# Kernel optimization log

Hardware: AMD Instinct MI355X
Metric: run time of the kernel (lower is better)

The kernel has to match this reference:

```python
import jax, jax.numpy as jnp
import numpy as np


def setup_inputs() -> dict:
    key = jax.random.key(0)
    k1, k2 = jax.random.split(key)
    B, D = 8192, 768
    M, K, dsub = 96, 256, 8  # subvector_num, 2**subvector_bits, emb_size // subvector_num
    vecs = jax.random.normal(k1, (B, D), dtype=jnp.float32)
    # matches nn.Parameter(...).uniform_(-0.1, 0.1)
    codebook = jax.random.uniform(k2, (M, K, dsub), dtype=jnp.float32, minval=-0.1, maxval=0.1)
    return {"vecs": vecs, "codebook": codebook}


def reference(vecs, codebook):
    B = vecs.shape[0]
    M, K, dsub = codebook.shape
    v = vecs.reshape(B, M, dsub)
    # code_selection: proba = -||v - c||^2, computed via expansion to avoid the
    # (B, M, K, dsub) broadcast intermediate: -(||v||^2 - 2 v.c + ||c||^2)
    v2 = jnp.sum(v * v, axis=-1, keepdims=True)       # (B, M, 1)
    c2 = jnp.sum(codebook * codebook, axis=-1)        # (M, K)
    vc = jnp.einsum('bmd,mkd->bmk', v, codebook)      # (B, M, K)
    proba = 2.0 * vc - v2 - c2[None]                  # (B, M, K)
    assign = jax.nn.softmax(proba, axis=-1)
    # STEstimator: hard one-hot forward, soft-assign gradient
    hard = jax.nn.one_hot(jnp.argmax(assign, axis=-1), K, dtype=assign.dtype)
    ste = assign + jax.lax.stop_gradient(hard - assign)
    # quantized_vecs: (B, M, 1, K) @ (M, K, dsub) -> (B, M, dsub) -> (B, D)
    q = jnp.einsum('bmk,mkd->bmd', ste, codebook)
    return q.reshape(B, M * dsub)
```

## Files before the change

### kernel.cpp

```cpp
#include <hip/hip_runtime.h>

namespace {
constexpr int kB = 8192;
constexpr int kD = 768;
constexpr int kM = 96;
constexpr int kK = 256;
constexpr int kDS = 8;
constexpr int kThreads = 256;
constexpr int kBPT = 4;
constexpr int kBT = kThreads * kBPT;
}

__device__ __forceinline__ float tree8_sq(float4 a, float4 b) {
    float q0 = __fmul_rn(a.x, a.x), q1 = __fmul_rn(a.y, a.y);
    float q2 = __fmul_rn(a.z, a.z), q3 = __fmul_rn(a.w, a.w);
    float q4 = __fmul_rn(b.x, b.x), q5 = __fmul_rn(b.y, b.y);
    float q6 = __fmul_rn(b.z, b.z), q7 = __fmul_rn(b.w, b.w);
    return __fadd_rn(__fadd_rn(__fadd_rn(q0, q1), __fadd_rn(q2, q3)),
                     __fadd_rn(__fadd_rn(q4, q5), __fadd_rn(q6, q7)));
}

__global__ __launch_bounds__(kThreads)
void pq_argmax_kernel(const float* __restrict__ vecs,
                      const float* __restrict__ cb,
                      float* __restrict__ out) {
    __shared__ float s_cb[kK * kDS];
    __shared__ float s_c2[kK];

    const int tid = threadIdx.x;
    const int m  = blockIdx.x % kM;
    const int bt = blockIdx.x / kM;

    {
        const float4* src = reinterpret_cast<const float4*>(cb) + (size_t)m * (kK * kDS / 4);
        float4 a = src[2 * tid + 0];
        float4 b = src[2 * tid + 1];
        reinterpret_cast<float4*>(s_cb)[2 * tid + 0] = a;
        reinterpret_cast<float4*>(s_cb)[2 * tid + 1] = b;
        s_c2[tid] = tree8_sq(a, b);
    }
    __syncthreads();

    const int b0 = bt * kBT + tid;

    float v[kBPT][kDS];
    float v2[kBPT];
#pragma unroll
    for (int j = 0; j < kBPT; ++j) {
        const float* vr = vecs + (size_t)(b0 + j * kThreads) * kD + m * kDS;
        float4 a = reinterpret_cast<const float4*>(vr)[0];
        float4 b = reinterpret_cast<const float4*>(vr)[1];
        v[j][0] = a.x; v[j][1] = a.y; v[j][2] = a.z; v[j][3] = a.w;
        v[j][4] = b.x; v[j][5] = b.y; v[j][6] = b.z; v[j][7] = b.w;
        v2[j] = tree8_sq(a, b);
    }

    float best[kBPT];
    int   bestk[kBPT];
#pragma unroll
    for (int j = 0; j < kBPT; ++j) { best[j] = -3.402823466e38f; bestk[j] = 0; }

#pragma unroll 4
    for (int k = 0; k < kK; ++k) {
        float4 ca  = reinterpret_cast<const float4*>(s_cb)[2 * k + 0];
        float4 cbv = reinterpret_cast<const float4*>(s_cb)[2 * k + 1];
        float  c2k = s_c2[k];
#pragma unroll
        for (int j = 0; j < kBPT; ++j) {
            float acc = __fmul_rn(v[j][0], ca.x);
            acc = __fadd_rn(acc, __fmul_rn(v[j][1], ca.y));
            acc = __fadd_rn(acc, __fmul_rn(v[j][2], ca.z));
            acc = __fadd_rn(acc, __fmul_rn(v[j][3], ca.w));
            acc = __fadd_rn(acc, __fmul_rn(v[j][4], cbv.x));
            acc = __fadd_rn(acc, __fmul_rn(v[j][5], cbv.y));
            acc = __fadd_rn(acc, __fmul_rn(v[j][6], cbv.z));
            acc = __fadd_rn(acc, __fmul_rn(v[j][7], cbv.w));
            float p = __fsub_rn(__fsub_rn(__fmul_rn(2.0f, acc), v2[j]), c2k);
            bool gt = p > best[j];
            best[j]  = gt ? p : best[j];
            bestk[j] = gt ? k : bestk[j];
        }
    }

#pragma unroll
    for (int j = 0; j < kBPT; ++j) {
        const float4* q = reinterpret_cast<const float4*>(s_cb) + 2 * bestk[j];
        float4* o = reinterpret_cast<float4*>(out + (size_t)(b0 + j * kThreads) * kD + m * kDS);
        o[0] = q[0];
        o[1] = q[1];
    }
}

extern "C" void kernel_launch(void* const* d_in, const int* in_sizes, int n_in,
                              void* d_out, int out_size, void* d_ws, size_t ws_size,
                              hipStream_t stream) {
    const float* vecs = (const float*)d_in[0];
    const float* cb   = (const float*)d_in[1];
    float* out = (float*)d_out;

    dim3 grid(kM * (kB / kBT));
    pq_argmax_kernel<<<grid, kThreads, 0, stream>>>(vecs, cb, out);
}
```

Baseline: 136.7 us.

## Compute code scores with fp16 split-precision MFMA and exact fp32 rescoring of near-ties

```diff
diff --git a/kernel.cpp b/kernel.cpp
--- a/kernel.cpp
+++ b/kernel.cpp
@@ -1,14 +1,20 @@
 #include <hip/hip_runtime.h>
+#include <hip/hip_fp16.h>
+
+typedef __attribute__((ext_vector_type(8))) _Float16 half8;
+typedef __attribute__((ext_vector_type(4))) float f32x4;
 
 namespace {
-constexpr int kB = 8192;
-constexpr int kD = 768;
-constexpr int kM = 96;
-constexpr int kK = 256;
-constexpr int kDS = 8;
+constexpr int kMsub = 96;
+constexpr int kK    = 256;
+constexpr int kDS   = 8;
+constexpr int kD    = 768;
 constexpr int kThreads = 256;
-constexpr int kBPT = 4;
-constexpr int kBT = kThreads * kBPT;
+constexpr int kWaves = 4;
+constexpr int kBPI  = 16;
+constexpr int kIters = 8;
+constexpr int kBPB  = kWaves * kBPI * kIters;
+constexpr float kEPS = 0.048f;
 }
 
 __device__ __forceinline__ float tree8_sq(float4 a, float4 b) {
@@ -20,74 +26,184 @@
                      __fadd_rn(__fadd_rn(q4, q5), __fadd_rn(q6, q7)));
 }
 
+__device__ __forceinline__ uint pkh(__half a, __half b) {
+    return (uint)__half_as_ushort(a) | ((uint)__half_as_ushort(b) << 16);
+}
+__device__ __forceinline__ uint pk2(float a, float b) {
+    return pkh(__float2half_rn(a), __float2half_rn(b));
+}
+union U4H8 { uint4 u; half8 h; };
+__device__ __forceinline__ half8 as_h8(uint4 u) { U4H8 x; x.u = u; return x.h; }
+
 __global__ __launch_bounds__(kThreads)
-void pq_argmax_kernel(const float* __restrict__ vecs,
-                      const float* __restrict__ cb,
-                      float* __restrict__ out) {
-    __shared__ float s_cb[kK * kDS];
-    __shared__ float s_c2[kK];
-
-    const int tid = threadIdx.x;
-    const int m  = blockIdx.x % kM;
-    const int bt = blockIdx.x / kM;
+void pq_mfma_kernel(const float* __restrict__ vecs,
+                    const float* __restrict__ cbg,
+                    float* __restrict__ out) {
+    __shared__ uint4  s_cbh[kK];
+    __shared__ uint4  s_cbl[kK];
+    __shared__ uint4  s_cbq[kK];
+    __shared__ uint   s_c2hl[kK];
+    __shared__ float  s_c2[kK];
+    __shared__ float4 s_cb[kK][2];
+    __shared__ float4 s_v[kWaves][kBPI][2];
+    __shared__ __align__(16) uint2 s_vh[kWaves][kBPI][2];
+    __shared__ __align__(16) uint2 s_vl[kWaves][kBPI][2];
+    __shared__ float s_v2[kWaves][kBPI];
+    __shared__ int   s_win[kWaves][kBPI];
+
+    const int tid  = threadIdx.x;
+    const int lane = tid & 63;
+    const int w    = tid >> 6;
+    const int m    = blockIdx.x % kMsub;
+    const int bt   = blockIdx.x / kMsub;
+    const int g    = lane >> 4;
+    const int c15  = lane & 15;
 
     {
-        const float4* src = reinterpret_cast<const float4*>(cb) + (size_t)m * (kK * kDS / 4);
-        float4 a = src[2 * tid + 0];
-        float4 b = src[2 * tid + 1];
-        reinterpret_cast<float4*>(s_cb)[2 * tid + 0] = a;
-        reinterpret_cast<float4*>(s_cb)[2 * tid + 1] = b;
-        s_c2[tid] = tree8_sq(a, b);
+        const int k = tid;
+        const float4* cr = reinterpret_cast<const float4*>(cbg + ((size_t)m * kK + k) * kDS);
+        float4 c0 = cr[0], c1 = cr[1];
+        s_cb[k][0] = c0; s_cb[k][1] = c1;
+        float c2 = tree8_sq(c0, c1);
+        s_c2[k] = c2;
+        float c2s = -128.0f * c2;
+        __half nh = __float2half_rn(c2s);
+        __half nl = __float2half_rn(c2s - __half2float(nh));
+        s_c2hl[k] = pkh(nh, nl);
+        float e[8] = {c0.x, c0.y, c0.z, c0.w, c1.x, c1.y, c1.z, c1.w};
+        uint hh[4], ll[4], qq[4];
+#pragma unroll
+        for (int i = 0; i < 4; ++i) {
+            float a = 256.0f * e[2*i], b = 256.0f * e[2*i+1];
+            __half ha = __float2half_rn(a), hb = __float2half_rn(b);
+            hh[i] = pkh(ha, hb);
+            ll[i] = pk2(a - __half2float(ha), b - __half2float(hb));
+            qq[i] = pk2(0.125f * e[2*i], 0.125f * e[2*i+1]);
+        }
+        s_cbh[k] = make_uint4(hh[0], hh[1], hh[2], hh[3]);
+        s_cbl[k] = make_uint4(ll[0], ll[1], ll[2], ll[3]);
+        s_cbq[k] = make_uint4(qq[0], qq[1], qq[2], qq[3]);
     }
     __syncthreads();
 
-    const int b0 = bt * kBT + tid;
-
-    float v[kBPT][kDS];
-    float v2[kBPT];
-#pragma unroll
-    for (int j = 0; j < kBPT; ++j) {
-        const float* vr = vecs + (size_t)(b0 + j * kThreads) * kD + m * kDS;
-        float4 a = reinterpret_cast<const float4*>(vr)[0];
-        float4 b = reinterpret_cast<const float4*>(vr)[1];
-        v[j][0] = a.x; v[j][1] = a.y; v[j][2] = a.z; v[j][3] = a.w;
-        v[j][4] = b.x; v[j][5] = b.y; v[j][6] = b.z; v[j][7] = b.w;
-        v2[j] = tree8_sq(a, b);
+    half8 A[16];
+#pragma unroll
+    for (int t = 0; t < 16; ++t) {
+        const int code = t * 16 + c15;
+        uint4 raw;
+        if (g == 0)      raw = s_cbh[code];
+        else if (g == 1) raw = s_cbl[code];
+        else if (g == 2) raw = s_cbq[code];
+        else             raw = make_uint4(s_c2hl[code], 0u, 0u, 0u);
+        A[t] = as_h8(raw);
     }
-
-    float best[kBPT];
-    int   bestk[kBPT];
-#pragma unroll
-    for (int j = 0; j < kBPT; ++j) { best[j] = -3.402823466e38f; bestk[j] = 0; }
-
-#pragma unroll 4
-    for (int k = 0; k < kK; ++k) {
-        float4 ca  = reinterpret_cast<const float4*>(s_cb)[2 * k + 0];
-        float4 cbv = reinterpret_cast<const float4*>(s_cb)[2 * k + 1];
-        float  c2k = s_c2[k];
-#pragma unroll
-        for (int j = 0; j < kBPT; ++j) {
-            float acc = __fmul_rn(v[j][0], ca.x);
-            acc = __fadd_rn(acc, __fmul_rn(v[j][1], ca.y));
-            acc = __fadd_rn(acc, __fmul_rn(v[j][2], ca.z));
-            acc = __fadd_rn(acc, __fmul_rn(v[j][3], ca.w));
-            acc = __fadd_rn(acc, __fmul_rn(v[j][4], cbv.x));
-            acc = __fadd_rn(acc, __fmul_rn(v[j][5], cbv.y));
-            acc = __fadd_rn(acc, __fmul_rn(v[j][6], cbv.z));
-            acc = __fadd_rn(acc, __fmul_rn(v[j][7], cbv.w));
-            float p = __fsub_rn(__fsub_rn(__fmul_rn(2.0f, acc), v2[j]), c2k);
-            bool gt = p > best[j];
-            best[j]  = gt ? p : best[j];
-            bestk[j] = gt ? k : bestk[j];
-        }
-    }
-
-#pragma unroll
-    for (int j = 0; j < kBPT; ++j) {
-        const float4* q = reinterpret_cast<const float4*>(s_cb) + 2 * bestk[j];
-        float4* o = reinterpret_cast<float4*>(out + (size_t)(b0 + j * kThreads) * kD + m * kDS);
-        o[0] = q[0];
-        o[1] = q[1];
+    const f32x4 zz = {0.0f, 0.0f, 0.0f, 0.0f};
+
+    for (int it = 0; it < kIters; ++it) {
+        const size_t bg0 = (size_t)bt * kBPB + (size_t)it * (kWaves * kBPI) + (size_t)w * kBPI;
+
+        float4 vown;
+        if (lane < 32) {
+            const int h = g;
+            const float4* vp = reinterpret_cast<const float4*>(
+                vecs + (bg0 + c15) * kD + (size_t)m * kDS) + h;
+            vown = *vp;
+            s_v[w][c15][h] = vown;
+            __half h0 = __float2half_rn(vown.x), h1 = __float2half_rn(vown.y);
+            __half h2 = __float2half_rn(vown.z), h3 = __float2half_rn(vown.w);
+            uint2 vhp = { pkh(h0, h1), pkh(h2, h3) };
+            uint2 vlp = { pk2(2048.0f * (vown.x - __half2float(h0)),
+                              2048.0f * (vown.y - __half2float(h1))),
+                          pk2(2048.0f * (vown.z - __half2float(h2)),
+                              2048.0f * (vown.w - __half2float(h3))) };
+            s_vh[w][c15][h] = vhp;
+            s_vl[w][c15][h] = vlp;
+        }
+        if (lane < 16) {
+            float4 vpart = s_v[w][c15][1];
+            s_v2[w][c15] = tree8_sq(vown, vpart);
+        }
+
+        half8 B;
+        {
+            uint4 raw;
+            if (g == 3) raw = make_uint4(0x3C003C00u, 0u, 0u, 0u);
+            else {
+                const uint4* p = (g == 2)
+                    ? reinterpret_cast<const uint4*>(&s_vl[w][c15][0])
+                    : reinterpret_cast<const uint4*>(&s_vh[w][c15][0]);
+                raw = *p;
+            }
+            B = as_h8(raw);
+        }
+        f32x4 D[16];
+#pragma unroll
+        for (int t = 0; t < 16; ++t)
+            D[t] = __builtin_amdgcn_mfma_f32_16x16x32_f16(A[t], B, zz, 0, 0, 0);
+
+        float m1 = -3.402823466e38f;
+#pragma unroll
+        for (int t = 0; t < 16; ++t)
+            m1 = fmaxf(m1, fmaxf(fmaxf(D[t].x, D[t].y), fmaxf(D[t].z, D[t].w)));
+        float gmax = fmaxf(m1, __shfl_xor(m1, 16));
+        gmax = fmaxf(gmax, __shfl_xor(gmax, 32));
+        const float thr = gmax - kEPS;
+
+        int cnt = 0, idx = 0;
+#pragma unroll
+        for (int t = 0; t < 16; ++t) {
+            { bool ge = D[t].x >= thr; cnt += ge ? 1 : 0; idx = ge ? (t*16 + g*4 + 0) : idx; }
+            { bool ge = D[t].y >= thr; cnt += ge ? 1 : 0; idx = ge ? (t*16 + g*4 + 1) : idx; }
+            { bool ge = D[t].z >= thr; cnt += ge ? 1 : 0; idx = ge ? (t*16 + g*4 + 2) : idx; }
+            { bool ge = D[t].w >= thr; cnt += ge ? 1 : 0; idx = ge ? (t*16 + g*4 + 3) : idx; }
+        }
+        int cnt4 = cnt + __shfl_xor(cnt, 16);
+        cnt4 += __shfl_xor(cnt4, 32);
+
+        if (cnt4 == 1) {
+            if (cnt == 1) s_win[w][c15] = idx;
+        } else {
+            float4 va = s_v[w][c15][0], vb = s_v[w][c15][1];
+            const float v2 = s_v2[w][c15];
+            float vr[8] = {va.x, va.y, va.z, va.w, vb.x, vb.y, vb.z, vb.w};
+            auto exactP = [&](int code) -> float {
+                float4 ca = s_cb[code][0], cc = s_cb[code][1];
+                float acc = __fmul_rn(vr[0], ca.x);
+                acc = __fadd_rn(acc, __fmul_rn(vr[1], ca.y));
+                acc = __fadd_rn(acc, __fmul_rn(vr[2], ca.z));
+                acc = __fadd_rn(acc, __fmul_rn(vr[3], ca.w));
+                acc = __fadd_rn(acc, __fmul_rn(vr[4], cc.x));
+                acc = __fadd_rn(acc, __fmul_rn(vr[5], cc.y));
+                acc = __fadd_rn(acc, __fmul_rn(vr[6], cc.z));
+                acc = __fadd_rn(acc, __fmul_rn(vr[7], cc.w));
+                return __fsub_rn(__fsub_rn(__fmul_rn(2.0f, acc), v2), s_c2[code]);
+            };
+            float bp = -3.402823466e38f; int bk = 1 << 30;
+            if (cnt == 1) {
+                bp = exactP(idx); bk = idx;
+            } else if (cnt >= 2) {
+#pragma unroll
+                for (int t = 0; t < 16; ++t) {
+                    if (D[t].x >= thr) { int c = t*16+g*4+0; float p = exactP(c); if (p > bp || (p == bp && c < bk)) { bp = p; bk = c; } }
+                    if (D[t].y >= thr) { int c = t*16+g*4+1; float p = exactP(c); if (p > bp || (p == bp && c < bk)) { bp = p; bk = c; } }
+                    if (D[t].z >= thr) { int c = t*16+g*4+2; float p = exactP(c); if (p > bp || (p == bp && c < bk)) { bp = p; bk = c; } }
+                    if (D[t].w >= thr) { int c = t*16+g*4+3; float p = exactP(c); if (p > bp || (p == bp && c < bk)) { bp = p; bk = c; } }
+                }
+            }
+            { float p2 = __shfl_xor(bp, 16); int k2 = __shfl_xor(bk, 16);
+              if (p2 > bp || (p2 == bp && k2 < bk)) { bp = p2; bk = k2; } }
+            { float p2 = __shfl_xor(bp, 32); int k2 = __shfl_xor(bk, 32);
+              if (p2 > bp || (p2 == bp && k2 < bk)) { bp = p2; bk = k2; } }
+            if (lane < 16) s_win[w][c15] = bk;
+        }
+
+        if (lane < 16) {
+            const int code = s_win[w][c15];
+            float4 q0 = s_cb[code][0], q1 = s_cb[code][1];
+            float4* op = reinterpret_cast<float4*>(out + (bg0 + c15) * kD + (size_t)m * kDS);
+            op[0] = q0;
+            op[1] = q1;
+        }
     }
 }
 
@@ -95,9 +211,9 @@
                               void* d_out, int out_size, void* d_ws, size_t ws_size,
                               hipStream_t stream) {
     const float* vecs = (const float*)d_in[0];
-    const float* cb   = (const float*)d_in[1];
+    const float* cbg  = (const float*)d_in[1];
     float* out = (float*)d_out;
 
-    dim3 grid(kM * (kB / kBT));
-    pq_argmax_kernel<<<grid, kThreads, 0, stream>>>(vecs, cb, out);
-}
+    dim3 grid(kMsub * (8192 / kBPB));
+    pq_mfma_kernel<<<grid, kThreads, 0, stream>>>(vecs, cbg, out);
+}
```

Measured after the change: 192.9 us. 1.41x slower.

## Use packed f32x2 math for two rows and read codebook via scalar loads

Applied to the files above, without the earlier changes.

```diff
diff --git a/kernel.cpp b/kernel.cpp
--- a/kernel.cpp
+++ b/kernel.cpp
@@ -1,14 +1,16 @@
 #include <hip/hip_runtime.h>
 
+typedef __attribute__((ext_vector_type(2))) float f32x2;
+
 namespace {
-constexpr int kB = 8192;
-constexpr int kD = 768;
-constexpr int kM = 96;
-constexpr int kK = 256;
+constexpr int kD  = 768;
+constexpr int kM  = 96;
+constexpr int kK  = 256;
 constexpr int kDS = 8;
-constexpr int kThreads = 256;
-constexpr int kBPT = 4;
-constexpr int kBT = kThreads * kBPT;
+constexpr int kThreads = 128;
+constexpr int kBPT = 8;
+constexpr int kBPB = kThreads * kBPT;
+constexpr int kB   = 8192;
 }
 
 __device__ __forceinline__ float tree8_sq(float4 a, float4 b) {
@@ -21,38 +23,44 @@
 }
 
 __global__ __launch_bounds__(kThreads)
-void pq_argmax_kernel(const float* __restrict__ vecs,
-                      const float* __restrict__ cb,
-                      float* __restrict__ out) {
-    __shared__ float s_cb[kK * kDS];
-    __shared__ float s_c2[kK];
+void pq_pk_kernel(const float* __restrict__ vecs,
+                  const float* __restrict__ cbg,
+                  float* __restrict__ out) {
+    #pragma clang fp contract(off)
+
+    __shared__ float  s_c2[kK];
+    __shared__ float4 s_cb[kK][2];
 
     const int tid = threadIdx.x;
-    const int m  = blockIdx.x % kM;
-    const int bt = blockIdx.x / kM;
+    const int m   = blockIdx.x % kM;
+    const int bt  = blockIdx.x / kM;
+    const float* __restrict__ cbm = cbg + (size_t)m * (kK * kDS);
 
-    {
-        const float4* src = reinterpret_cast<const float4*>(cb) + (size_t)m * (kK * kDS / 4);
-        float4 a = src[2 * tid + 0];
-        float4 b = src[2 * tid + 1];
-        reinterpret_cast<float4*>(s_cb)[2 * tid + 0] = a;
-        reinterpret_cast<float4*>(s_cb)[2 * tid + 1] = b;
-        s_c2[tid] = tree8_sq(a, b);
+    for (int r = tid; r < kK; r += kThreads) {
+        const float4* cr = reinterpret_cast<const float4*>(cbm + r * kDS);
+        float4 c0 = cr[0], c1 = cr[1];
+        s_cb[r][0] = c0; s_cb[r][1] = c1;
+        s_c2[r] = tree8_sq(c0, c1);
     }
     __syncthreads();
 
-    const int b0 = bt * kBT + tid;
-
-    float v[kBPT][kDS];
-    float v2[kBPT];
+    const size_t b0 = (size_t)bt * kBPB + tid;
+    f32x2 vv[kBPT / 2][kDS];
+    f32x2 v2p[kBPT / 2];
 #pragma unroll
-    for (int j = 0; j < kBPT; ++j) {
-        const float* vr = vecs + (size_t)(b0 + j * kThreads) * kD + m * kDS;
-        float4 a = reinterpret_cast<const float4*>(vr)[0];
-        float4 b = reinterpret_cast<const float4*>(vr)[1];
-        v[j][0] = a.x; v[j][1] = a.y; v[j][2] = a.z; v[j][3] = a.w;
-        v[j][4] = b.x; v[j][5] = b.y; v[j][6] = b.z; v[j][7] = b.w;
-        v2[j] = tree8_sq(a, b);
+    for (int p = 0; p < kBPT / 2; ++p) {
+#pragma unroll
+        for (int h = 0; h < 2; ++h) {
+            const int j = 2 * p + h;
+            const float* vr = vecs + (b0 + (size_t)j * kThreads) * kD + m * kDS;
+            float4 a = reinterpret_cast<const float4*>(vr)[0];
+            float4 c = reinterpret_cast<const float4*>(vr)[1];
+            v2p[p][h] = tree8_sq(a, c);
+            vv[p][0][h] = 2.0f * a.x; vv[p][1][h] = 2.0f * a.y;
+            vv[p][2][h] = 2.0f * a.z; vv[p][3][h] = 2.0f * a.w;
+            vv[p][4][h] = 2.0f * c.x; vv[p][5][h] = 2.0f * c.y;
+            vv[p][6][h] = 2.0f * c.z; vv[p][7][h] = 2.0f * c.w;
+        }
     }
 
     float best[kBPT];
@@ -60,34 +68,41 @@
 #pragma unroll
     for (int j = 0; j < kBPT; ++j) { best[j] = -3.402823466e38f; bestk[j] = 0; }
 
-#pragma unroll 4
+#pragma unroll 2
     for (int k = 0; k < kK; ++k) {
-        float4 ca  = reinterpret_cast<const float4*>(s_cb)[2 * k + 0];
-        float4 cbv = reinterpret_cast<const float4*>(s_cb)[2 * k + 1];
-        float  c2k = s_c2[k];
+        const float* cr = cbm + k * kDS;
+        const float c0 = cr[0], c1 = cr[1], c2 = cr[2], c3 = cr[3];
+        const float c4 = cr[4], c5 = cr[5], c6 = cr[6], c7 = cr[7];
+        const float n2 = s_c2[k];
 #pragma unroll
-        for (int j = 0; j < kBPT; ++j) {
-            float acc = __fmul_rn(v[j][0], ca.x);
-            acc = __fadd_rn(acc, __fmul_rn(v[j][1], ca.y));
-            acc = __fadd_rn(acc, __fmul_rn(v[j][2], ca.z));
-            acc = __fadd_rn(acc, __fmul_rn(v[j][3], ca.w));
-            acc = __fadd_rn(acc, __fmul_rn(v[j][4], cbv.x));
-            acc = __fadd_rn(acc, __fmul_rn(v[j][5], cbv.y));
-            acc = __fadd_rn(acc, __fmul_rn(v[j][6], cbv.z));
-            acc = __fadd_rn(acc, __fmul_rn(v[j][7], cbv.w));
-            float p = __fsub_rn(__fsub_rn(__fmul_rn(2.0f, acc), v2[j]), c2k);
-            bool gt = p > best[j];
-            best[j]  = gt ? p : best[j];
-            bestk[j] = gt ? k : bestk[j];
+        for (int p = 0; p < kBPT / 2; ++p) {
+            f32x2 acc = vv[p][0] * c0;
+            acc = acc + vv[p][1] * c1;
+            acc = acc + vv[p][2] * c2;
+            acc = acc + vv[p][3] * c3;
+            acc = acc + vv[p][4] * c4;
+            acc = acc + vv[p][5] * c5;
+            acc = acc + vv[p][6] * c6;
+            acc = acc + vv[p][7] * c7;
+            f32x2 pr = (acc - v2p[p]) - n2;
+            const int j0 = 2 * p, j1 = 2 * p + 1;
+            { bool gt = pr[0] > best[j0];
+              best[j0]  = gt ? pr[0] : best[j0];
+              bestk[j0] = gt ? k : bestk[j0]; }
+            { bool gt = pr[1] > best[j1];
+              best[j1]  = gt ? pr[1] : best[j1];
+              bestk[j1] = gt ? k : bestk[j1]; }
         }
     }
 
 #pragma unroll
     for (int j = 0; j < kBPT; ++j) {
-        const float4* q = reinterpret_cast<const float4*>(s_cb) + 2 * bestk[j];
-        float4* o = reinterpret_cast<float4*>(out + (size_t)(b0 + j * kThreads) * kD + m * kDS);
-        o[0] = q[0];
-        o[1] = q[1];
+        const int kk = bestk[j];
+        float4 q0 = s_cb[kk][0], q1 = s_cb[kk][1];
+        float4* op = reinterpret_cast<float4*>(
+            out + (b0 + (size_t)j * kThreads) * kD + m * kDS);
+        op[0] = q0;
+        op[1] = q1;
     }
 }
 
@@ -95,9 +110,9 @@
                               void* d_out, int out_size, void* d_ws, size_t ws_size,
                               hipStream_t stream) {
     const float* vecs = (const float*)d_in[0];
-    const float* cb   = (const float*)d_in[1];
+    const float* cbg  = (const float*)d_in[1];
     float* out = (float*)d_out;
 
-    dim3 grid(kM * (kB / kBT));
-    pq_argmax_kernel<<<grid, kThreads, 0, stream>>>(vecs, cb, out);
+    dim3 grid(kM * (kB / kBPB));
+    pq_pk_kernel<<<grid, kThreads, 0, stream>>>(vecs, cbg, out);
 }
```

Result: slower. 209.3 us (+53.1%).

## Vectorize distance dot products with packed f32x2 math over two rows

Applied to the files above, without the earlier changes.

```diff
diff --git a/kernel.cpp b/kernel.cpp
--- a/kernel.cpp
+++ b/kernel.cpp
@@ -1,14 +1,16 @@
 #include <hip/hip_runtime.h>
 
+typedef __attribute__((ext_vector_type(2))) float f32x2;
+
 namespace {
-constexpr int kB = 8192;
-constexpr int kD = 768;
-constexpr int kM = 96;
-constexpr int kK = 256;
+constexpr int kB  = 8192;
+constexpr int kD  = 768;
+constexpr int kM  = 96;
+constexpr int kK  = 256;
 constexpr int kDS = 8;
 constexpr int kThreads = 256;
-constexpr int kBPT = 4;
-constexpr int kBT = kThreads * kBPT;
+constexpr int kBPT = 2;
+constexpr int kBT  = kThreads * kBPT;
 }
 
 __device__ __forceinline__ float tree8_sq(float4 a, float4 b) {
@@ -21,73 +23,72 @@
 }
 
 __global__ __launch_bounds__(kThreads)
-void pq_argmax_kernel(const float* __restrict__ vecs,
-                      const float* __restrict__ cb,
-                      float* __restrict__ out) {
-    __shared__ float s_cb[kK * kDS];
-    __shared__ float s_c2[kK];
+void pq_pk2_kernel(const float* __restrict__ vecs,
+                   const float* __restrict__ cbg,
+                   float* __restrict__ out) {
+    #pragma clang fp contract(off)
+
+    __shared__ float  s_c2[kK];
+    __shared__ float4 s_cb[kK][2];
 
     const int tid = threadIdx.x;
-    const int m  = blockIdx.x % kM;
-    const int bt = blockIdx.x / kM;
+    const int m   = blockIdx.x % kM;
+    const int bt  = blockIdx.x / kM;
 
     {
-        const float4* src = reinterpret_cast<const float4*>(cb) + (size_t)m * (kK * kDS / 4);
+        const float4* src = reinterpret_cast<const float4*>(cbg) + (size_t)m * (kK * kDS / 4);
         float4 a = src[2 * tid + 0];
         float4 b = src[2 * tid + 1];
-        reinterpret_cast<float4*>(s_cb)[2 * tid + 0] = a;
-        reinterpret_cast<float4*>(s_cb)[2 * tid + 1] = b;
+        s_cb[tid][0] = a; s_cb[tid][1] = b;
         s_c2[tid] = tree8_sq(a, b);
     }
     __syncthreads();
 
-    const int b0 = bt * kBT + tid;
-
-    float v[kBPT][kDS];
-    float v2[kBPT];
+    const size_t b0 = (size_t)bt * kBT + tid;
+    f32x2 vv[kDS];
+    f32x2 v2;
 #pragma unroll
-    for (int j = 0; j < kBPT; ++j) {
-        const float* vr = vecs + (size_t)(b0 + j * kThreads) * kD + m * kDS;
+    for (int h = 0; h < 2; ++h) {
+        const float* vr = vecs + (b0 + (size_t)h * kThreads) * kD + m * kDS;
         float4 a = reinterpret_cast<const float4*>(vr)[0];
-        float4 b = reinterpret_cast<const float4*>(vr)[1];
-        v[j][0] = a.x; v[j][1] = a.y; v[j][2] = a.z; v[j][3] = a.w;
-        v[j][4] = b.x; v[j][5] = b.y; v[j][6] = b.z; v[j][7] = b.w;
-        v2[j] = tree8_sq(a, b);
+        float4 c = reinterpret_cast<const float4*>(vr)[1];
+        v2[h] = tree8_sq(a, c);
+        vv[0][h] = 2.0f * a.x; vv[1][h] = 2.0f * a.y;
+        vv[2][h] = 2.0f * a.z; vv[3][h] = 2.0f * a.w;
+        vv[4][h] = 2.0f * c.x; vv[5][h] = 2.0f * c.y;
+        vv[6][h] = 2.0f * c.z; vv[7][h] = 2.0f * c.w;
     }
 
-    float best[kBPT];
-    int   bestk[kBPT];
-#pragma unroll
-    for (int j = 0; j < kBPT; ++j) { best[j] = -3.402823466e38f; bestk[j] = 0; }
+    float best0 = -3.402823466e38f, best1 = -3.402823466e38f;
+    int   bk0 = 0, bk1 = 0;
 
 #pragma unroll 4
     for (int k = 0; k < kK; ++k) {
-        float4 ca  = reinterpret_cast<const float4*>(s_cb)[2 * k + 0];
-        float4 cbv = reinterpret_cast<const float4*>(s_cb)[2 * k + 1];
-        float  c2k = s_c2[k];
-#pragma unroll
-        for (int j = 0; j < kBPT; ++j) {
-            float acc = __fmul_rn(v[j][0], ca.x);
-            acc = __fadd_rn(acc, __fmul_rn(v[j][1], ca.y));
-            acc = __fadd_rn(acc, __fmul_rn(v[j][2], ca.z));
-            acc = __fadd_rn(acc, __fmul_rn(v[j][3], ca.w));
-            acc = __fadd_rn(acc, __fmul_rn(v[j][4], cbv.x));
-            acc = __fadd_rn(acc, __fmul_rn(v[j][5], cbv.y));
-            acc = __fadd_rn(acc, __fmul_rn(v[j][6], cbv.z));
-            acc = __fadd_rn(acc, __fmul_rn(v[j][7], cbv.w));
-            float p = __fsub_rn(__fsub_rn(__fmul_rn(2.0f, acc), v2[j]), c2k);
-            bool gt = p > best[j];
-            best[j]  = gt ? p : best[j];
-            bestk[j] = gt ? k : bestk[j];
-        }
+        const float4 ca = s_cb[k][0];
+        const float4 cb4 = s_cb[k][1];
+        const float  n2 = s_c2[k];
+        f32x2 acc = vv[0] * ca.x;
+        acc = acc + vv[1] * ca.y;
+        acc = acc + vv[2] * ca.z;
+        acc = acc + vv[3] * ca.w;
+        acc = acc + vv[4] * cb4.x;
+        acc = acc + vv[5] * cb4.y;
+        acc = acc + vv[6] * cb4.z;
+        acc = acc + vv[7] * cb4.w;
+        f32x2 pr = (acc - v2) - n2;
+        { bool gt = pr[0] > best0; best0 = gt ? pr[0] : best0; bk0 = gt ? k : bk0; }
+        { bool gt = pr[1] > best1; best1 = gt ? pr[1] : best1; bk1 = gt ? k : bk1; }
     }
 
-#pragma unroll
-    for (int j = 0; j < kBPT; ++j) {
-        const float4* q = reinterpret_cast<const float4*>(s_cb) + 2 * bestk[j];
-        float4* o = reinterpret_cast<float4*>(out + (size_t)(b0 + j * kThreads) * kD + m * kDS);
-        o[0] = q[0];
-        o[1] = q[1];
+    {
+        float4 q0 = s_cb[bk0][0], q1 = s_cb[bk0][1];
+        float4* op = reinterpret_cast<float4*>(out + b0 * kD + m * kDS);
+        op[0] = q0; op[1] = q1;
+    }
+    {
+        float4 q0 = s_cb[bk1][0], q1 = s_cb[bk1][1];
+        float4* op = reinterpret_cast<float4*>(out + (b0 + kThreads) * kD + m * kDS);
+        op[0] = q0; op[1] = q1;
     }
 }
 
@@ -95,9 +96,9 @@
                               void* d_out, int out_size, void* d_ws, size_t ws_size,
                               hipStream_t stream) {
     const float* vecs = (const float*)d_in[0];
-    const float* cb   = (const float*)d_in[1];
+    const float* cbg  = (const float*)d_in[1];
     float* out = (float*)d_out;
 
     dim3 grid(kM * (kB / kBT));
-    pq_argmax_kernel<<<grid, kThreads, 0, stream>>>(vecs, cb, out);
+    pq_pk2_kernel<<<grid, kThreads, 0, stream>>>(vecs, cbg, out);
 }
```

Result: slower. 152.5 us (+11.5%).
